# Performance work log

Measured on AMD Instinct MI355X. Metric: run time of the kernel, lower is better.

The kernel has to match this reference:

```python
import math
import jax, jax.numpy as jnp
import numpy as np

B, HRV, WRV, CRV = 1, 32, 512, 64
CBEV, HB, WB = 128, 256, 256
D, COUT, K, HEADS, P = 128, 128, 5, 8, 6
HD = D // HEADS
NBINS = 110
RMAX, BIN = 55.0, 0.5
XMIN, XMAX, YMIN, YMAX = -55.0, 55.0, -55.0, 55.0

_ELEV = np.array([-30.67, -29.33, -28.0, -26.66, -25.33, -24.0, -22.67, -21.33,
                  -20.0, -18.67, -17.33, -16.0, -14.67, -13.33, -12.0, -10.67,
                  -9.33, -8.0, -6.66, -5.33, -4.0, -2.67, -1.33, 0.0, 1.33,
                  2.67, 4.0, 5.33, 6.67, 8.0, 9.33, 10.67], dtype=np.float32)

def _make_uvec():
    az_line = np.linspace(-math.pi, math.pi, WRV + 1, dtype=np.float32)[:-1]
    az = az_line + 0.5 * (az_line[1] - az_line[0])
    elev = np.deg2rad(_ELEV[::-1].reshape(HRV, -1).mean(axis=1)).astype(np.float32)
    az2 = np.broadcast_to(az[None, :], (HRV, WRV))
    el2 = np.broadcast_to(elev[:, None], (HRV, WRV))
    ux = np.cos(az2) * np.cos(el2)
    uy = np.sin(az2) * np.cos(el2)
    uz = np.broadcast_to(np.sin(el2), (HRV, WRV))
    return jnp.asarray(ux), jnp.asarray(uy), jnp.asarray(uz)

_UX, _UY, _UZ = _make_uvec()

def _lin(x, w, b):
    # 1x1 conv / Linear: w is torch-layout [Cout, Cin]
    return jnp.einsum('...c,oc->...o', x, w) + b

def _gn(x, gamma, beta, groups, eps=1e-5):
    Bn, H, W, C = x.shape
    xg = x.reshape(Bn, H, W, groups, C // groups)
    mu = xg.mean(axis=(1, 2, 4), keepdims=True)
    var = ((xg - mu) ** 2).mean(axis=(1, 2, 4), keepdims=True)
    xg = (xg - mu) * jax.lax.rsqrt(var + eps)
    return xg.reshape(Bn, H, W, C) * gamma + beta

def _gelu(x):
    return jax.nn.gelu(x, approximate=False)

def _conv3x3_circ(x, w):
    # torch Conv2d(3x3, padding=1, padding_mode='circular', bias=False)
    xp = jnp.pad(x, ((0, 0), (1, 1), (1, 1), (0, 0)), mode='wrap')
    k = jnp.transpose(w, (2, 3, 1, 0))  # OIHW -> HWIO
    return jax.lax.conv_general_dilated(xp, k, (1, 1), 'VALID',
                                        dimension_numbers=('NHWC', 'HWIO', 'NHWC'))

def _deform_sample(v, loc, aw):
    # v: [B, HB*WB, HEADS, HD]; loc: [B,Nq,HEADS,P,2] normalized; aw: [B,Nq,HEADS,P]
    # Emulates grid_sample(bilinear, zeros padding, align_corners=False).
    Bq = v.shape[0]
    vflat = jnp.transpose(v, (0, 2, 1, 3))       # [B, H, HW, hd]
    loc_t = jnp.transpose(loc, (0, 2, 1, 3, 4))  # [B, H, Nq, P, 2]
    aw_t = jnp.transpose(aw, (0, 2, 1, 3))       # [B, H, Nq, P]
    x = loc_t[..., 0] * WB - 0.5
    y = loc_t[..., 1] * HB - 0.5
    x0 = jnp.floor(x); y0 = jnp.floor(y)
    wx1 = x - x0; wy1 = y - y0
    x0i = x0.astype(jnp.int32); y0i = y0.astype(jnp.int32)
    gather = jax.vmap(jax.vmap(lambda vf, idx: vf[idx]))  # over B, heads
    def corner(xi, yi, wgt, acc):
        valid = (xi >= 0) & (xi < WB) & (yi >= 0) & (yi < HB)
        idx = jnp.clip(yi, 0, HB - 1) * WB + jnp.clip(xi, 0, WB - 1)
        g = gather(vflat, idx)  # [B, H, Nq, P, hd]
        return acc + g * (wgt * valid.astype(g.dtype))[..., None]
    acc = jnp.zeros(x.shape + (HD,), dtype=v.dtype)
    acc = corner(x0i,     y0i,     (1 - wx1) * (1 - wy1), acc)
    acc = corner(x0i + 1, y0i,     wx1 * (1 - wy1), acc)
    acc = corner(x0i,     y0i + 1, (1 - wx1) * wy1, acc)
    acc = corner(x0i + 1, y0i + 1, wx1 * wy1, acc)
    out = (acc * aw_t[..., None]).sum(axis=3)    # [B, H, Nq, hd]
    return jnp.transpose(out, (0, 2, 1, 3)).reshape(Bq, -1, D)

def _forward(x_rv, bev, lidar2ego_mat, wq, bq, wv, bv, wo, bo,
             qd_w1, qd_b1, qd_w2, qd_b2,
             rh_w1, rh_b1, rh_g1, rh_be1, rh_w2, rh_g2, rh_be2, rh_w3, rh_b3,
             off_w, off_b, aw_w, aw_b, vp_w, vp_b, op_w, op_b):
    Bq = x_rv.shape[0]
    Q0 = _lin(x_rv, wq, bq)                                   # [B,Hrv,Wrv,D]
    Vmap = _lin(jnp.transpose(bev, (0, 2, 3, 1)), wv, bv)     # [B,HB,WB,D]
    uvec = jnp.broadcast_to(jnp.stack([_UX, _UY, _UZ], axis=-1)[None], (Bq, HRV, WRV, 3))
    h = _gelu(_gn(_lin(jnp.concatenate([x_rv, uvec], axis=-1), rh_w1, rh_b1), rh_g1, rh_be1, 8))
    h = _gelu(_gn(_conv3x3_circ(h, rh_w2), rh_g2, rh_be2, 8))
    depth_logits = _lin(h, rh_w3, rh_b3)                      # [B,Hrv,Wrv,NBINS]
    depth_dist = jax.nn.softmax(depth_logits, axis=-1)
    topk_prob, topk_idx = jax.lax.top_k(depth_dist, K)        # [B,Hrv,Wrv,K]
    topk_depths = jnp.minimum(BIN * (topk_idx.astype(jnp.float32) + 0.5), RMAX - 0.5 * BIN)
    xl = topk_depths * _UX[None, :, :, None]
    yl = topk_depths * _UY[None, :, :, None]
    zl = topk_depths * _UZ[None, :, :, None]
    p = jnp.stack([xl, yl, zl, jnp.ones_like(xl)], axis=-1)   # [B,Hrv,Wrv,K,4]
    pe = jnp.einsum('bhwki,ij->bhwkj', p, lidar2ego_mat[0])
    rx = (pe[..., 0] - XMIN) / (XMAX - XMIN)
    ry = (pe[..., 1] - YMIN) / (YMAX - YMIN)
    ref_pts = jnp.stack([jnp.clip(rx, 0.0, 1.0), jnp.clip(ry, 0.0, 1.0)], axis=-1).reshape(Bq, -1, 2)
    qin = jnp.concatenate([jnp.broadcast_to(Q0[:, :, :, None, :], (Bq, HRV, WRV, K, D)),
                           (topk_depths / RMAX)[..., None]], axis=-1)
    query = _lin(_gelu(_lin(qin, qd_w1, qd_b1)), qd_w2, qd_b2).reshape(Bq, -1, D)
    value = Vmap.reshape(Bq, -1, D)
    # --- MSDA (mmcv MultiScaleDeformableAttention, 1 level) ---
    v = _lin(value, vp_w, vp_b).reshape(Bq, -1, HEADS, HD)
    Nq = query.shape[1]
    off = _lin(query, off_w, off_b).reshape(Bq, Nq, HEADS, P, 2)
    aw = jax.nn.softmax(_lin(query, aw_w, aw_b).reshape(Bq, Nq, HEADS, P), axis=-1)
    loc = ref_pts[:, :, None, None, :] + off / jnp.array([WB, HB], dtype=jnp.float32)
    y_msda = _lin(_deform_sample(v, loc, aw), op_w, op_b) + query  # residual add
    y_msda = y_msda.reshape(Bq, HRV, WRV, K, D)
    wgt = topk_prob / (topk_prob.sum(axis=-1, keepdims=True) + 1e-8)
    y = (y_msda * wgt[..., None]).sum(axis=3)
    y = _lin(y, wo, bo)                                       # [B,Hrv,Wrv,COUT]
    return y, jnp.transpose(depth_logits, (0, 3, 1, 2))

def setup_inputs():
    key = jax.random.key(0)
    ks = jax.random.split(key, 32)
    def rn(i, shape, s):
        return jax.random.normal(ks[i], shape, dtype=jnp.float32) * s
    return dict(
        x_rv=rn(0, (B, HRV, WRV, CRV), 1.0),
        bev=rn(1, (B, CBEV, HB, WB), 1.0),
        lidar2ego_mat=jnp.eye(4, dtype=jnp.float32)[None] + rn(2, (1, 4, 4), 0.01),
        wq=rn(3, (D, CRV), 0.05), bq=rn(4, (D,), 0.01),
        wv=rn(5, (D, CBEV), 0.05), bv=rn(6, (D,), 0.01),
        wo=rn(7, (COUT, D), 0.05), bo=rn(8, (COUT,), 0.01),
        qd_w1=rn(9, (D, D + 1), 0.05), qd_b1=rn(10, (D,), 0.01),
        qd_w2=rn(11, (D, D), 0.05), qd_b2=rn(12, (D,), 0.01),
        rh_w1=rn(13, (128, CRV + 3), 0.05), rh_b1=rn(14, (128,), 0.01),
        rh_g1=jnp.ones((128,), jnp.float32), rh_be1=jnp.zeros((128,), jnp.float32),
        rh_w2=rn(15, (64, 128, 3, 3), 0.05),
        rh_g2=jnp.ones((64,), jnp.float32), rh_be2=jnp.zeros((64,), jnp.float32),
        rh_w3=rn(16, (NBINS, 64), 0.05), rh_b3=rn(17, (NBINS,), 0.01),
        off_w=rn(18, (HEADS * P * 2, D), 0.02), off_b=rn(19, (HEADS * P * 2,), 2.0),
        aw_w=rn(20, (HEADS * P, D), 0.02), aw_b=rn(21, (HEADS * P,), 0.01),
        vp_w=rn(22, (D, D), 0.05), vp_b=rn(23, (D,), 0.01),
        op_w=rn(24, (D, D), 0.05), op_b=rn(25, (D,), 0.01),
    )

def reference(x_rv, bev, lidar2ego_mat, wq, bq, wv, bv, wo, bo,
              qd_w1, qd_b1, qd_w2, qd_b2,
              rh_w1, rh_b1, rh_g1, rh_be1, rh_w2, rh_g2, rh_be2, rh_w3, rh_b3,
              off_w, off_b, aw_w, aw_b, vp_w, vp_b, op_w, op_b):
    return _forward(x_rv, bev, lidar2ego_mat, wq, bq, wv, bv, wo, bo,
                    qd_w1, qd_b1, qd_w2, qd_b2,
                    rh_w1, rh_b1, rh_g1, rh_be1, rh_w2, rh_g2, rh_be2, rh_w3, rh_b3,
                    off_w, off_b, aw_w, aw_b, vp_w, vp_b, op_w, op_b)
```

## Files before the change

kernel.cpp:

```cpp
#include <hip/hip_runtime.h>
#include <math.h>

#define NT 256

typedef unsigned short u16;
typedef unsigned int u32;
typedef _Float16 f16;
typedef __attribute__((ext_vector_type(2))) unsigned int u32x2;
typedef __attribute__((ext_vector_type(4))) unsigned int u32x4;
typedef __attribute__((ext_vector_type(4))) float f32x4;
typedef __attribute__((ext_vector_type(8))) short s16x8;
typedef __attribute__((ext_vector_type(8))) _Float16 f16x8;

namespace {

__device__ const float c_elev[32] = {
  -30.67f,-29.33f,-28.0f,-26.66f,-25.33f,-24.0f,-22.67f,-21.33f,
  -20.0f,-18.67f,-17.33f,-16.0f,-14.67f,-13.33f,-12.0f,-10.67f,
  -9.33f,-8.0f,-6.66f,-5.33f,-4.0f,-2.67f,-1.33f,0.0f,1.33f,
  2.67f,4.0f,5.33f,6.67f,8.0f,9.33f,10.67f };

__device__ __forceinline__ float gelu_f(float x) {
  return 0.5f * x * (1.0f + erff(x * 0.70710678118654752440f));
}
__device__ __forceinline__ u16 bf16rne(float f) {
  u32 u = __builtin_bit_cast(u32, f);
  u32 r = u + 0x7FFFu + ((u >> 16) & 1u);
  return (u16)(r >> 16);
}
__device__ __forceinline__ float bf2f(u16 h) {
  u32 u = ((u32)h) << 16;
  return __builtin_bit_cast(float, u);
}
__device__ __forceinline__ u32 packsplit(float x) {
  f16 h = (f16)x;
  f16 l = (f16)(x - (float)h);
  return (u32)__builtin_bit_cast(u16, h) | ((u32)__builtin_bit_cast(u16, l) << 16);
}
__device__ __forceinline__ void unpack16(u32x4 a, u32x4 b, f16x8& hi, f16x8& lo) {
  u32x4 h, l;
  h[0] = (a[0] & 0xFFFFu) | (a[1] << 16);  l[0] = (a[0] >> 16) | (a[1] & 0xFFFF0000u);
  h[1] = (a[2] & 0xFFFFu) | (a[3] << 16);  l[1] = (a[2] >> 16) | (a[3] & 0xFFFF0000u);
  h[2] = (b[0] & 0xFFFFu) | (b[1] << 16);  l[2] = (b[0] >> 16) | (b[1] & 0xFFFF0000u);
  h[3] = (b[2] & 0xFFFFu) | (b[3] << 16);  l[3] = (b[2] >> 16) | (b[3] & 0xFFFF0000u);
  hi = __builtin_bit_cast(f16x8, h);
  lo = __builtin_bit_cast(f16x8, l);
}

template<int COREAL, int CO, int KPAD, int CI, int PROD, int AMODE, bool DOGELU, bool OBF>
__global__ __launch_bounds__(NT)
void slin(const float* __restrict__ Af, const float* __restrict__ A2,
          const u32* __restrict__ Wp, const float* __restrict__ bias,
          float* __restrict__ outF, u16* __restrict__ outB)
{
  constexpr int BM = 64;
  constexpr int NFR = CO / 16;
  constexpr int KS = KPAD / 32;
  __shared__ u32 lds[BM * KPAD];
  const int tid = threadIdx.x;
  const long row0 = (long)blockIdx.x * BM;

  for (int i = tid; i < BM * (KPAD / 4); i += NT) {
    int r = i / (KPAD / 4), c = (i % (KPAD / 4)) * 4;
    long pix = row0 + r;
    u32x4 o;
    if constexpr (AMODE == 0) {
      if (c + 3 < CI) {
        f32x4 v = *(const f32x4*)(Af + pix * CI + c);
#pragma unroll
        for (int e = 0; e < 4; e++) o[e] = packsplit(v[e]);
      } else {
#pragma unroll
        for (int e = 0; e < 4; e++) {
          int cc = c + e;
          o[e] = packsplit(cc < CI ? Af[pix * CI + cc] : 0.f);
        }
      }
    } else {
      if (c + 3 < 64) {
        f32x4 v = *(const f32x4*)(Af + pix * 64 + c);
#pragma unroll
        for (int e = 0; e < 4; e++) o[e] = packsplit(v[e]);
      } else {
#pragma unroll
        for (int e = 0; e < 4; e++) {
          int cc = c + e;
          float x = (cc < 64) ? Af[pix * 64 + cc] : ((cc < 67) ? A2[pix * 3 + cc - 64] : 0.f);
          o[e] = packsplit(x);
        }
      }
    }
    *(u32x4*)((char*)lds + (((r * KPAD + c) * 4) ^ ((r & 7) << 4))) = o;
  }
  __syncthreads();

  const int wave = tid >> 6, lane = tid & 63;
  const int mb = wave * 16;
  const int lr = lane & 15, kq = lane >> 4;

  f32x4 acc[NFR] = {};
#pragma unroll
  for (int ks = 0; ks < KS; ks++) {
    const int arow = mb + lr;
    const u32 sw = (arow & 7) << 4;
    const int base = arow * KPAD * 4 + ks * 128 + kq * 32;
    u32x4 a0 = *(const u32x4*)((char*)lds + (base ^ sw));
    u32x4 a1 = *(const u32x4*)((char*)lds + ((base + 16) ^ sw));
    f16x8 ah, al;
    unpack16(a0, a1, ah, al);
#pragma unroll
    for (int nf = 0; nf < NFR; nf++) {
      const u32* wp = Wp + (nf * 16 + lr) * KPAD + ks * 32 + kq * 8;
      u32x4 w0 = *(const u32x4*)wp;
      u32x4 w1 = *(const u32x4*)(wp + 4);
      f16x8 wh, wl;
      unpack16(w0, w1, wh, wl);
      acc[nf] = __builtin_amdgcn_mfma_f32_16x16x32_f16(ah, wh, acc[nf], 0, 0, 0);
      if constexpr (PROD == 3) {
        acc[nf] = __builtin_amdgcn_mfma_f32_16x16x32_f16(ah, wl, acc[nf], 0, 0, 0);
        acc[nf] = __builtin_amdgcn_mfma_f32_16x16x32_f16(al, wh, acc[nf], 0, 0, 0);
      }
    }
  }

#pragma unroll
  for (int nf = 0; nf < NFR; nf++) {
    int col = nf * 16 + lr;
    if (col >= COREAL) continue;
    float bcol = bias[col];
#pragma unroll
    for (int r = 0; r < 4; r++) {
      long row = row0 + mb + kq * 4 + r;
      float val = acc[nf][r] + bcol;
      if constexpr (DOGELU) val = gelu_f(val);
      if constexpr (OBF) outB[row * COREAL + col] = bf16rne(val);
      else               outF[row * COREAL + col] = val;
    }
  }
}

__global__ __launch_bounds__(NT)
void conv_mfma(const float* __restrict__ X, const u32* __restrict__ Wc,
               float* __restrict__ Y)
{
  __shared__ u32 lds[4 * 18 * 128];
  const int tid = threadIdx.x;
  const int bRow = (blockIdx.x >> 5) * 2;
  const int bCol = (blockIdx.x & 31) * 16;

  for (int i = tid; i < 4 * 18 * 32; i += NT) {
    int c4 = (i & 31) * 4;
    int col = (i >> 5) % 18;
    int row = i / (18 * 32);
    int gy = (bRow + row - 1 + 32) & 31;
    int gx = (bCol + col - 1 + 512) & 511;
    f32x4 v = *(const f32x4*)(X + ((long)gy * 512 + gx) * 128 + c4);
    u32x4 o;
#pragma unroll
    for (int e = 0; e < 4; e++) o[e] = packsplit(v[e]);
    *(u32x4*)((char*)lds + ((((row * 18 + col) * 128 + c4) * 4) ^ ((col & 7) << 4))) = o;
  }
  __syncthreads();

  const int wave = tid >> 6, lane = tid & 63;
  const int wm = wave >> 1;
  const int nb = (wave & 1) * 32;
  const int lr = lane & 15, kq = lane >> 4;

  f32x4 acc[2] = {};
  for (int t = 0; t < 9; t++) {
    const int ky = t / 3, kx = t % 3;
    const int wrow = wm + ky;
    const int wcol = lr + kx;
    const u32 sw = (wcol & 7) << 4;
    const int rowbase = (wrow * 18 + wcol) * 512;
#pragma unroll
    for (int ks = 0; ks < 4; ks++) {
      const int base = rowbase + ks * 128 + kq * 32;
      u32x4 a0 = *(const u32x4*)((char*)lds + (base ^ sw));
      u32x4 a1 = *(const u32x4*)((char*)lds + ((base + 16) ^ sw));
      f16x8 ah, al;
      unpack16(a0, a1, ah, al);
#pragma unroll
      for (int nf = 0; nf < 2; nf++) {
        const u32* wp = Wc + ((t * 64 + nb + nf * 16 + lr) * 128 + ks * 32 + kq * 8);
        u32x4 w0 = *(const u32x4*)wp;
        u32x4 w1 = *(const u32x4*)(wp + 4);
        f16x8 wh, wl;
        unpack16(w0, w1, wh, wl);
        acc[nf] = __builtin_amdgcn_mfma_f32_16x16x32_f16(ah, wh, acc[nf], 0, 0, 0);
        acc[nf] = __builtin_amdgcn_mfma_f32_16x16x32_f16(ah, wl, acc[nf], 0, 0, 0);
        acc[nf] = __builtin_amdgcn_mfma_f32_16x16x32_f16(al, wh, acc[nf], 0, 0, 0);
      }
    }
  }

  const int gy = bRow + wm;
#pragma unroll
  for (int nf = 0; nf < 2; nf++) {
    int co = nb + nf * 16 + lr;
#pragma unroll
    for (int r = 0; r < 4; r++) {
      int gx = bCol + kq * 4 + r;
      Y[((long)gy * 512 + gx) * 64 + co] = acc[nf][r];
    }
  }
}

template<int CO, int AMODE, bool DEPTH, bool DOGELU, bool RESID, bool WF, bool WBF>
__global__ __launch_bounds__(NT)
void mfma_lin(const void* __restrict__ Ap, const float* __restrict__ A2,
              const u16* __restrict__ Wb, const float* __restrict__ bias,
              const float* __restrict__ extraW, const u16* __restrict__ residB,
              float* __restrict__ outF, u16* __restrict__ outB, int ldA)
{
  constexpr int BM = 64;
  __shared__ u32x4 smem[(BM + CO) * 16];
  char* As = (char*)smem;
  char* Bs = (char*)smem + BM * 256;
  const int tid = threadIdx.x;
  const long row0 = (long)blockIdx.x * BM;

  for (int i = tid; i < CO * 16; i += NT) {
    int r = i >> 4, ck = i & 15;
    u32x4 v = ((const u32x4*)(Wb + r * 128))[ck];
    *(u32x4*)(Bs + ((r * 256 + ck * 16) ^ ((r & 7) << 4))) = v;
  }
  if constexpr (AMODE == 0 || AMODE == 1) {
    const u16* A = (const u16*)Ap;
    for (int i = tid; i < BM * 16; i += NT) {
      int r = i >> 4, ck = i & 15;
      long src = (AMODE == 1) ? ((row0 + r) / 5) : (row0 + r);
      u32x4 v = ((const u32x4*)(A + src * 128))[ck];
      *(u32x4*)(As + ((r * 256 + ck * 16) ^ ((r & 7) << 4))) = v;
    }
  } else if constexpr (AMODE == 3) {
    const u16* A = (const u16*)Ap;
    for (int i = tid; i < BM * 16; i += NT) {
      int r = i >> 4, ck = i & 15;
      long q = row0 + r;
      float s[8];
#pragma unroll
      for (int e = 0; e < 8; e++) s[e] = 0.f;
#pragma unroll
      for (int j = 0; j < 5; j++) {
        float w = A2[q * 5 + j];
        u32x4 v = ((const u32x4*)(A + (q * 5 + j) * 128))[ck];
        const u16* hv = (const u16*)&v;
#pragma unroll
        for (int e = 0; e < 8; e++) s[e] += w * bf2f(hv[e]);
      }
      u32x4 o;
#pragma unroll
      for (int e = 0; e < 4; e++)
        o[e] = (u32)bf16rne(s[2 * e]) | ((u32)bf16rne(s[2 * e + 1]) << 16);
      *(u32x4*)(As + ((r * 256 + ck * 16) ^ ((r & 7) << 4))) = o;
    }
  } else if constexpr (AMODE == 4) {
    const float* A = (const float*)Ap;
    for (int i = tid; i < 128 * 16; i += NT) {
      int k = i >> 4, rg = i & 15;
      f32x4 v = *(const f32x4*)(A + (long)k * ldA + row0 + rg * 4);
#pragma unroll
      for (int e = 0; e < 4; e++) {
        int r = rg * 4 + e;
        *(u16*)(As + ((r * 256 + k * 2) ^ ((r & 7) << 4))) = bf16rne(v[e]);
      }
    }
  }
  __syncthreads();

  constexpr int WROWS = (CO >= 96) ? 2 : 4;
  constexpr int WCOLS = 4 / WROWS;
  constexpr int MW = BM / WROWS;
  constexpr int NW = CO / WCOLS;
  constexpr int MFR = MW / 16;
  constexpr int NFR = NW / 16;
  const int wave = tid >> 6, lane = tid & 63;
  const int wm = wave / WCOLS, wn = wave % WCOLS;
  const int mb = wm * MW, nb = wn * NW;
  const int lr = lane & 15, kq = lane >> 4;

  f32x4 acc[MFR][NFR] = {};
#pragma unroll
  for (int ks = 0; ks < 4; ks++) {
    const int kof = (ks * 32 + kq * 8) * 2;
    s16x8 af[MFR], bfr[NFR];
#pragma unroll
    for (int mf = 0; mf < MFR; mf++) {
      int r = mb + mf * 16 + lr;
      af[mf] = *(const s16x8*)(As + ((r * 256 + kof) ^ ((r & 7) << 4)));
    }
#pragma unroll
    for (int nf = 0; nf < NFR; nf++) {
      int r = nb + nf * 16 + lr;
      bfr[nf] = *(const s16x8*)(Bs + ((r * 256 + kof) ^ ((r & 7) << 4)));
    }
#pragma unroll
    for (int mf = 0; mf < MFR; mf++)
#pragma unroll
      for (int nf = 0; nf < NFR; nf++)
        acc[mf][nf] = __builtin_amdgcn_mfma_f32_16x16x32_bf16(af[mf], bfr[nf], acc[mf][nf], 0, 0, 0);
  }

#pragma unroll
  for (int mf = 0; mf < MFR; mf++) {
#pragma unroll
    for (int nf = 0; nf < NFR; nf++) {
      const int col = nb + nf * 16 + lr;
      const float bcol = bias[col];
      float ew = 0.f;
      if constexpr (DEPTH) ew = extraW[col];
#pragma unroll
      for (int r = 0; r < 4; r++) {
        long row = row0 + mb + mf * 16 + kq * 4 + r;
        float val = acc[mf][nf][r] + bcol;
        if constexpr (DEPTH) val += ew * (A2[row] * (1.0f / 55.0f));
        if constexpr (RESID) val += bf2f(residB[row * 128 + col]);
        if constexpr (DOGELU) val = gelu_f(val);
        if constexpr (WF) outF[row * CO + col] = val;
        if constexpr (WBF) outB[row * CO + col] = bf16rne(val);
      }
    }
  }
}

__global__ void wcomb_kernel(const float* __restrict__ vp_w, const float* __restrict__ wv,
                             const float* __restrict__ vp_b, const float* __restrict__ bv,
                             u16* __restrict__ wc, float* __restrict__ bc)
{
  int o = blockIdx.x;
  int c = threadIdx.x;
  float s = 0.f;
  for (int m = 0; m < 128; m++) s += vp_w[o * 128 + m] * wv[m * 128 + c];
  wc[o * 128 + c] = bf16rne(s);
  if (c == 0) {
    float b = vp_b[o];
    for (int m = 0; m < 128; m++) b += vp_w[o * 128 + m] * bv[m];
    bc[o] = b;
  }
}

__global__ void cvtw_kernel(const float* __restrict__ qd_w1, const float* __restrict__ qd_w2,
                            const float* __restrict__ off_w, const float* __restrict__ aw_w,
                            const float* __restrict__ op_w, const float* __restrict__ wo,
                            u16* Wq1, u16* Wq2, u16* Woff, u16* Waw, u16* Wop, u16* Wwo,
                            float* w1last)
{
  int i = blockIdx.x * NT + threadIdx.x;
  if (i < 16384) {
    int r = i >> 7, c = i & 127;
    Wq1[i] = bf16rne(qd_w1[r * 129 + c]);
    Wq2[i] = bf16rne(qd_w2[i]);
    Wop[i] = bf16rne(op_w[i]);
    Wwo[i] = bf16rne(wo[i]);
  }
  if (i < 12288) Woff[i] = bf16rne(off_w[i]);
  if (i < 6144)  Waw[i]  = bf16rne(aw_w[i]);
  if (i < 128)   w1last[i] = qd_w1[i * 129 + 128];
}

__global__ void packw_kernel(const float* __restrict__ rh_w1, const float* __restrict__ rh_w3,
                             const float* __restrict__ wq, const float* __restrict__ rh_w2,
                             u32* Wh1, u32* Wlog, u32* Wq0, u32* Wcv)
{
  int i = blockIdx.x * NT + threadIdx.x;
  if (i < 128 * 96) {
    int r = i / 96, c = i % 96;
    Wh1[i] = packsplit(c < 67 ? rh_w1[r * 67 + c] : 0.f);
  }
  if (i < 112 * 64) {
    int r = i / 64, c = i % 64;
    Wlog[i] = packsplit(r < 110 ? rh_w3[r * 64 + c] : 0.f);
  }
  if (i < 128 * 64) Wq0[i] = packsplit(wq[i]);
  if (i < 9 * 64 * 128) {
    int t = i / (64 * 128), o = (i / 128) % 64, c = i % 128;
    Wcv[i] = packsplit(rh_w2[(o * 128 + c) * 9 + t]);
  }
}

__global__ void uvec_kernel(float* __restrict__ uvec)
{
  int pix = blockIdx.x * NT + threadIdx.x;
  if (pix >= 16384) return;
  int hr = pix >> 9;
  int w = pix & 511;
  float el = c_elev[31 - hr] * 0.017453292519943295f;
  float az = -3.14159265358979323846f + ((float)w + 0.5f) * (6.283185307179586477f / 512.0f);
  float ce = cosf(el);
  uvec[pix * 3 + 0] = cosf(az) * ce;
  uvec[pix * 3 + 1] = sinf(az) * ce;
  uvec[pix * 3 + 2] = sinf(el);
}

template<int C, int S>
__global__ __launch_bounds__(NT)
void gn_stats_kernel(const float* __restrict__ X, int Npix, float* __restrict__ gs)
{
  constexpr int PPB = NT / C;
  int tid = threadIdx.x;
  int c = tid % C;
  int psub = tid / C;
  float sum = 0.f, ss = 0.f;
  for (long pix = (long)blockIdx.x * PPB + psub; pix < Npix; pix += (long)gridDim.x * PPB) {
    float v = X[pix * C + c];
    sum += v; ss += v * v;
  }
  __shared__ float ls[8][2];
  if (tid < 16) ls[tid / 2][tid % 2] = 0.f;
  __syncthreads();
  int g = c / S;
  atomicAdd(&ls[g][0], sum);
  atomicAdd(&ls[g][1], ss);
  __syncthreads();
  if (tid < 16) atomicAdd(&gs[tid], ls[tid / 2][tid % 2]);
}

template<int C, int S>
__global__ void gn_apply_kernel(float* __restrict__ X, long total, int Npix,
                                const float* __restrict__ gs,
                                const float* __restrict__ gamma, const float* __restrict__ beta)
{
  float cnt = (float)Npix * (float)S;
  for (long i = (long)blockIdx.x * NT + threadIdx.x; i < total; i += (long)gridDim.x * NT) {
    int c = (int)(i % C);
    int g = c / S;
    float mu = gs[g * 2] / cnt;
    float var = gs[g * 2 + 1] / cnt - mu * mu;
    float v = (X[i] - mu) * rsqrtf(var + 1e-5f);
    v = v * gamma[c] + beta[c];
    X[i] = gelu_f(v);
  }
}

__global__ __launch_bounds__(NT)
void tlogits_kernel(const float* __restrict__ logits, float* __restrict__ out1)
{
  __shared__ float ls[128][111];
  int p0 = blockIdx.x * 128;
  for (int i = threadIdx.x; i < 128 * 110; i += NT) {
    int p = i / 110, c = i % 110;
    ls[p][c] = logits[(long)(p0 + p) * 110 + c];
  }
  __syncthreads();
  for (int i = threadIdx.x; i < 110 * 128; i += NT) {
    int c = i / 128, p = i % 128;
    out1[(long)c * 16384 + p0 + p] = ls[p][c];
  }
}

__global__ __launch_bounds__(NT)
void topk_kernel(const float* __restrict__ logits, float* __restrict__ depths,
                 float* __restrict__ wgt)
{
  int lane = threadIdx.x & 63;
  int pix = (blockIdx.x * NT + threadIdx.x) >> 6;
  const float* lr = logits + (long)pix * 110;
  float v0 = (lane < 110) ? lr[lane] : -1e30f;
  float v1 = (lane + 64 < 110) ? lr[lane + 64] : -1e30f;
  float m = fmaxf(v0, v1);
#pragma unroll
  for (int s = 32; s; s >>= 1) m = fmaxf(m, __shfl_xor(m, s));
  float ex = ((lane < 110) ? expf(v0 - m) : 0.f) + ((lane + 64 < 110) ? expf(v1 - m) : 0.f);
  float den = ex;
#pragma unroll
  for (int s = 32; s; s >>= 1) den += __shfl_xor(den, s);
  float pr[5]; int pi[5];
#pragma unroll
  for (int j = 0; j < 5; j++) {
    float bv; int bi;
    if (v0 >= v1) { bv = v0; bi = lane; } else { bv = v1; bi = lane + 64; }
    for (int s = 1; s < 64; s <<= 1) {
      float ov = __shfl_xor(bv, s);
      int oi = __shfl_xor(bi, s);
      if (ov > bv || (ov == bv && oi < bi)) { bv = ov; bi = oi; }
    }
    pr[j] = expf(bv - m) / den;
    pi[j] = bi;
    if (bi == lane) v0 = -1e30f;
    if (bi == lane + 64) v1 = -1e30f;
  }
  if (lane == 0) {
    float tot = pr[0] + pr[1] + pr[2] + pr[3] + pr[4] + 1e-8f;
#pragma unroll
    for (int j = 0; j < 5; j++) {
      depths[pix * 5 + j] = fminf(0.5f * ((float)pi[j] + 0.5f), 54.75f);
      wgt[pix * 5 + j] = pr[j] / tot;
    }
  }
}

__global__ void refq_kernel(const float* __restrict__ depths, const float* __restrict__ uvec,
                            const float* __restrict__ L44, float* __restrict__ refq)
{
  long q = (long)blockIdx.x * NT + threadIdx.x;
  if (q >= 81920) return;
  long pix = q / 5;
  float d = depths[q];
  float px = d * uvec[pix * 3 + 0];
  float py = d * uvec[pix * 3 + 1];
  float pz = d * uvec[pix * 3 + 2];
  float pex = px * L44[0] + py * L44[4] + pz * L44[8] + L44[12];
  float pey = px * L44[1] + py * L44[5] + pz * L44[9] + L44[13];
  float rx = (pex + 55.0f) / 110.0f;
  float ry = (pey + 55.0f) / 110.0f;
  refq[q * 2 + 0] = fminf(fmaxf(rx, 0.f), 1.f);
  refq[q * 2 + 1] = fminf(fmaxf(ry, 0.f), 1.f);
}

__global__ __launch_bounds__(NT)
void msda_kernel(const u16* __restrict__ V, const float* __restrict__ refq,
                 const float* __restrict__ offb, const u16* __restrict__ awb,
                 u16* __restrict__ S)
{
  const int tid = threadIdx.x;
  const int kk = blockIdx.x >> 11;
  const int pg = blockIdx.x & 2047;
  const long pix = (long)pg * 8 + (tid >> 5);
  const long q = pix * 5 + kk;
  const int h = (tid >> 2) & 7;
  const int t4 = tid & 3;
  const int c0 = h * 16 + t4 * 4;
  const float rx = refq[q * 2 + 0], ry = refq[q * 2 + 1];
  const u16* ap = awb + q * 48 + h * 6;
  float a[6];
#pragma unroll
  for (int p = 0; p < 6; p++) a[p] = bf2f(ap[p]);
  float mx = fmaxf(fmaxf(fmaxf(a[0], a[1]), fmaxf(a[2], a[3])), fmaxf(a[4], a[5]));
  float se = 0.f;
#pragma unroll
  for (int p = 0; p < 6; p++) { a[p] = expf(a[p] - mx); se += a[p]; }
  float inv = 1.0f / se;
  const float* op = offb + q * 96 + h * 12;
  float acc0 = 0.f, acc1 = 0.f, acc2 = 0.f, acc3 = 0.f;
#pragma unroll
  for (int p = 0; p < 6; p++) {
    float x = (rx + op[p * 2 + 0] * (1.0f / 256.0f)) * 256.0f - 0.5f;
    float y = (ry + op[p * 2 + 1] * (1.0f / 256.0f)) * 256.0f - 0.5f;
    float x0f = floorf(x), y0f = floorf(y);
    float wx = x - x0f, wy = y - y0f;
    int x0 = (int)x0f, y0 = (int)y0f;
    float aw = a[p] * inv;
    float s0 = 0.f, s1 = 0.f, s2 = 0.f, s3 = 0.f;
#pragma unroll
    for (int cy = 0; cy < 2; cy++) {
#pragma unroll
      for (int cx = 0; cx < 2; cx++) {
        int xi = x0 + cx, yi = y0 + cy;
        float w = (cx ? wx : 1.f - wx) * (cy ? wy : 1.f - wy);
        bool valid = ((unsigned)xi < 256u) && ((unsigned)yi < 256u);
        int xc = min(max(xi, 0), 255), yc = min(max(yi, 0), 255);
        u32x2 v = *(const u32x2*)(V + (yc * 256 + xc) * 128 + c0);
        float w2 = valid ? w : 0.f;
        s0 += w2 * bf2f((u16)v[0]);
        s1 += w2 * bf2f((u16)(v[0] >> 16));
        s2 += w2 * bf2f((u16)v[1]);
        s3 += w2 * bf2f((u16)(v[1] >> 16));
      }
    }
    acc0 += aw * s0; acc1 += aw * s1; acc2 += aw * s2; acc3 += aw * s3;
  }
  u32x2 o;
  o[0] = (u32)bf16rne(acc0) | ((u32)bf16rne(acc1) << 16);
  o[1] = (u32)bf16rne(acc2) | ((u32)bf16rne(acc3) << 16);
  *(u32x2*)(S + q * 128 + c0) = o;
}

}

extern "C" void kernel_launch(void* const* d_in, const int* in_sizes, int n_in,
                              void* d_out, int out_size, void* d_ws, size_t ws_size,
                              hipStream_t stream)
{
  (void)in_sizes; (void)n_in; (void)out_size; (void)ws_size;
  const float* x_rv   = (const float*)d_in[0];
  const float* bev    = (const float*)d_in[1];
  const float* L44    = (const float*)d_in[2];
  const float* wq     = (const float*)d_in[3];
  const float* bq     = (const float*)d_in[4];
  const float* wv     = (const float*)d_in[5];
  const float* bv     = (const float*)d_in[6];
  const float* woW    = (const float*)d_in[7];
  const float* boB    = (const float*)d_in[8];
  const float* qd_w1  = (const float*)d_in[9];
  const float* qd_b1  = (const float*)d_in[10];
  const float* qd_w2  = (const float*)d_in[11];
  const float* qd_b2  = (const float*)d_in[12];
  const float* rh_w1  = (const float*)d_in[13];
  const float* rh_b1  = (const float*)d_in[14];
  const float* rh_g1  = (const float*)d_in[15];
  const float* rh_be1 = (const float*)d_in[16];
  const float* rh_w2  = (const float*)d_in[17];
  const float* rh_g2  = (const float*)d_in[18];
  const float* rh_be2 = (const float*)d_in[19];
  const float* rh_w3  = (const float*)d_in[20];
  const float* rh_b3  = (const float*)d_in[21];
  const float* off_w  = (const float*)d_in[22];
  const float* off_b  = (const float*)d_in[23];
  const float* aw_w   = (const float*)d_in[24];
  const float* aw_b   = (const float*)d_in[25];
  const float* vp_w   = (const float*)d_in[26];
  const float* vp_b   = (const float*)d_in[27];
  const float* op_w   = (const float*)d_in[28];
  const float* op_b   = (const float*)d_in[29];

  float* outY = (float*)d_out;
  float* outL = (float*)d_out + 2097152;

  char* wsb = (char*)d_ws;
  size_t off = 0;
  auto alloc = [&](size_t bytes) -> char* {
    char* p = wsb + off;
    off += (bytes + 255) & ~(size_t)255;
    return p;
  };

  u16*   wcomb  = (u16*)alloc(32768);
  float* bcomb  = (float*)alloc(512);
  float* uvec   = (float*)alloc(196608);
  float* stats  = (float*)alloc(128);
  float* depths = (float*)alloc(327680);
  float* wgtb   = (float*)alloc(327680);
  float* refqb  = (float*)alloc(655360);
  float* w1last = (float*)alloc(512);
  u16*   Wq1    = (u16*)alloc(32768);
  u16*   Wq2    = (u16*)alloc(32768);
  u16*   Wop    = (u16*)alloc(32768);
  u16*   Wwo    = (u16*)alloc(32768);
  u16*   Woff   = (u16*)alloc(24576);
  u16*   Waw    = (u16*)alloc(12288);
  u32*   Wh1    = (u32*)alloc(49152);
  u32*   Wlog   = (u32*)alloc(28672);
  u32*   Wq0    = (u32*)alloc(32768);
  u32*   Wcv    = (u32*)alloc(294912);
  char*  S1     = alloc(20971520);
  char*  S2     = alloc(4194304);
  char*  S3     = alloc(16777216);
  char*  S4     = alloc(20971520);
  char*  S5     = alloc(20971520);
  float* offbuf = (float*)alloc(31457280);
  u16*   awbf   = (u16*)alloc(7864320);

  float* h1buf  = (float*)S1;
  float* logits = (float*)(S1 + 8388608);
  float* h2buf  = (float*)(S1 + 15597568);
  u16*   smp    = (u16*)S1;
  u16*   Q0bf   = (u16*)S2;
  u16*   vbuf   = (u16*)S3;
  u16*   q1bf   = (u16*)S4;
  u16*   msdabf = (u16*)S4;
  u16*   querybf= (u16*)S5;

  float* stats1 = stats;
  float* stats2 = stats + 16;

  hipMemsetAsync((void*)stats, 0, 128, stream);

  wcomb_kernel<<<128, 128, 0, stream>>>(vp_w, wv, vp_b, bv, wcomb, bcomb);
  uvec_kernel<<<64, NT, 0, stream>>>(uvec);
  cvtw_kernel<<<64, NT, 0, stream>>>(qd_w1, qd_w2, off_w, aw_w, op_w, woW,
                                     Wq1, Wq2, Woff, Waw, Wop, Wwo, w1last);
  packw_kernel<<<288, NT, 0, stream>>>(rh_w1, rh_w3, wq, rh_w2, Wh1, Wlog, Wq0, Wcv);

  slin<128, 128, 64, 64, 1, 0, false, true><<<256, NT, 0, stream>>>(
      x_rv, nullptr, Wq0, bq, nullptr, Q0bf);

  slin<128, 128, 96, 67, 3, 1, false, false><<<256, NT, 0, stream>>>(
      x_rv, uvec, Wh1, rh_b1, h1buf, nullptr);
  gn_stats_kernel<128, 16><<<512, NT, 0, stream>>>(h1buf, 16384, stats1);
  gn_apply_kernel<128, 16><<<2048, NT, 0, stream>>>(h1buf, 16384L * 128, 16384, stats1, rh_g1, rh_be1);
  conv_mfma<<<512, NT, 0, stream>>>(h1buf, Wcv, h2buf);
  gn_stats_kernel<64, 8><<<512, NT, 0, stream>>>(h2buf, 16384, stats2);
  gn_apply_kernel<64, 8><<<1024, NT, 0, stream>>>(h2buf, 16384L * 64, 16384, stats2, rh_g2, rh_be2);
  slin<110, 112, 64, 64, 3, 0, false, false><<<256, NT, 0, stream>>>(
      h2buf, nullptr, Wlog, rh_b3, logits, nullptr);
  tlogits_kernel<<<128, NT, 0, stream>>>(logits, outL);
  topk_kernel<<<4096, NT, 0, stream>>>(logits, depths, wgtb);
  refq_kernel<<<320, NT, 0, stream>>>(depths, uvec, L44, refqb);

  mfma_lin<128, 4, false, false, false, false, true><<<1024, NT, 0, stream>>>(
      bev, nullptr, wcomb, bcomb, nullptr, nullptr, nullptr, vbuf, 65536);

  mfma_lin<128, 1, true, true, false, false, true><<<1280, NT, 0, stream>>>(
      Q0bf, depths, Wq1, qd_b1, w1last, nullptr, nullptr, q1bf, 0);
  mfma_lin<128, 0, false, false, false, false, true><<<1280, NT, 0, stream>>>(
      q1bf, nullptr, Wq2, qd_b2, nullptr, nullptr, nullptr, querybf, 0);

  mfma_lin<96, 0, false, false, false, true, false><<<1280, NT, 0, stream>>>(
      querybf, nullptr, Woff, off_b, nullptr, nullptr, offbuf, nullptr, 0);
  mfma_lin<48, 0, false, false, false, false, true><<<1280, NT, 0, stream>>>(
      querybf, nullptr, Waw, aw_b, nullptr, nullptr, nullptr, awbf, 0);

  msda_kernel<<<10240, NT, 0, stream>>>(vbuf, refqb, offbuf, awbf, smp);

  mfma_lin<128, 0, false, false, true, false, true><<<1280, NT, 0, stream>>>(
      smp, nullptr, Wop, op_b, nullptr, querybf, nullptr, msdabf, 0);

  mfma_lin<128, 3, false, false, false, true, false><<<256, NT, 0, stream>>>(
      msdabf, wgtb, Wwo, boB, nullptr, nullptr, outY, nullptr, 0);
}
```

Baseline: 430.8 us.

## Merge offset/attn GEMMs, fold output proj into final GEMM, widen MSDA threads

Merges the offset and attention-weight projections into one 160-column GEMM with a split epilogue. It uses linearity to move the weighted 5-candidate reduction ahead of the output projection. The op_w·wo product is precomputed, and a single K=256 GEMM over the concatenated reduced samples and query replaces two full-size GEMMs. The MSDA kernel now has each thread handle 16 channels of one head with 128-bit loads. The aim is fewer launches and less intermediate traffic, at the cost of changed bf16 rounding order and more registers per thread in MSDA.

```diff
diff --git a/kernel.cpp b/kernel.cpp
--- a/kernel.cpp
+++ b/kernel.cpp
@@ -31,6 +31,12 @@
 __device__ __forceinline__ float bf2f(u16 h) {
   u32 u = ((u32)h) << 16;
   return __builtin_bit_cast(float, u);
+}
+__device__ __forceinline__ float bflo(u32 v) {
+  return __builtin_bit_cast(float, v << 16);
+}
+__device__ __forceinline__ float bfhi(u32 v) {
+  return __builtin_bit_cast(float, v & 0xFFFF0000u);
 }
 __device__ __forceinline__ u32 packsplit(float x) {
   f16 h = (f16)x;
@@ -207,11 +213,11 @@
   }
 }
 
-template<int CO, int AMODE, bool DEPTH, bool DOGELU, bool RESID, bool WF, bool WBF>
+template<int CO, int AMODE, bool DEPTH, bool DOGELU, bool WF, bool WBF, bool SPLIT>
 __global__ __launch_bounds__(NT)
 void mfma_lin(const void* __restrict__ Ap, const float* __restrict__ A2,
               const u16* __restrict__ Wb, const float* __restrict__ bias,
-              const float* __restrict__ extraW, const u16* __restrict__ residB,
+              const float* __restrict__ extraW,
               float* __restrict__ outF, u16* __restrict__ outB, int ldA)
 {
   constexpr int BM = 64;
@@ -233,28 +239,6 @@
       long src = (AMODE == 1) ? ((row0 + r) / 5) : (row0 + r);
       u32x4 v = ((const u32x4*)(A + src * 128))[ck];
       *(u32x4*)(As + ((r * 256 + ck * 16) ^ ((r & 7) << 4))) = v;
-    }
-  } else if constexpr (AMODE == 3) {
-    const u16* A = (const u16*)Ap;
-    for (int i = tid; i < BM * 16; i += NT) {
-      int r = i >> 4, ck = i & 15;
-      long q = row0 + r;
-      float s[8];
-#pragma unroll
-      for (int e = 0; e < 8; e++) s[e] = 0.f;
-#pragma unroll
-      for (int j = 0; j < 5; j++) {
-        float w = A2[q * 5 + j];
-        u32x4 v = ((const u32x4*)(A + (q * 5 + j) * 128))[ck];
-        const u16* hv = (const u16*)&v;
-#pragma unroll
-        for (int e = 0; e < 8; e++) s[e] += w * bf2f(hv[e]);
-      }
-      u32x4 o;
-#pragma unroll
-      for (int e = 0; e < 4; e++)
-        o[e] = (u32)bf16rne(s[2 * e]) | ((u32)bf16rne(s[2 * e + 1]) << 16);
-      *(u32x4*)(As + ((r * 256 + ck * 16) ^ ((r & 7) << 4))) = o;
     }
   } else if constexpr (AMODE == 4) {
     const float* A = (const float*)Ap;
@@ -316,13 +300,95 @@
         long row = row0 + mb + mf * 16 + kq * 4 + r;
         float val = acc[mf][nf][r] + bcol;
         if constexpr (DEPTH) val += ew * (A2[row] * (1.0f / 55.0f));
-        if constexpr (RESID) val += bf2f(residB[row * 128 + col]);
         if constexpr (DOGELU) val = gelu_f(val);
-        if constexpr (WF) outF[row * CO + col] = val;
-        if constexpr (WBF) outB[row * CO + col] = bf16rne(val);
+        if constexpr (SPLIT) {
+          if (col < 96) outF[row * 96 + col] = val;
+          else if (col < 144) outB[row * 48 + (col - 96)] = bf16rne(val);
+        } else {
+          if constexpr (WF) outF[row * CO + col] = val;
+          if constexpr (WBF) outB[row * CO + col] = bf16rne(val);
+        }
       }
     }
   }
+}
+
+__global__ __launch_bounds__(NT)
+void final_gemm(const u16* __restrict__ A, const u16* __restrict__ Wc,
+                const float* __restrict__ cvec, float* __restrict__ outY)
+{
+  __shared__ char As[64 * 512];
+  const int tid = threadIdx.x;
+  const long row0 = (long)blockIdx.x * 64;
+  for (int i = tid; i < 64 * 32; i += NT) {
+    int r = i >> 5, ck = i & 31;
+    u32x4 v = ((const u32x4*)(A + (row0 + r) * 256))[ck];
+    *(u32x4*)(As + ((r * 512 + ck * 16) ^ ((r & 7) << 4))) = v;
+  }
+  __syncthreads();
+  const int wave = tid >> 6, lane = tid & 63;
+  const int mb = wave * 16;
+  const int lr = lane & 15, kq = lane >> 4;
+  f32x4 acc[8] = {};
+#pragma unroll
+  for (int ks = 0; ks < 8; ks++) {
+    const int kof = (ks * 32 + kq * 8) * 2;
+    const int r = mb + lr;
+    s16x8 af = *(const s16x8*)(As + ((r * 512 + kof) ^ ((r & 7) << 4)));
+#pragma unroll
+    for (int nf = 0; nf < 8; nf++) {
+      s16x8 bfr = *(const s16x8*)(Wc + (nf * 16 + lr) * 256 + ks * 32 + kq * 8);
+      acc[nf] = __builtin_amdgcn_mfma_f32_16x16x32_bf16(af, bfr, acc[nf], 0, 0, 0);
+    }
+  }
+#pragma unroll
+  for (int nf = 0; nf < 8; nf++) {
+    int col = nf * 16 + lr;
+    float bcol = cvec[col];
+#pragma unroll
+    for (int r = 0; r < 4; r++) {
+      long row = row0 + mb + kq * 4 + r;
+      outY[row * 128 + col] = acc[nf][r] + bcol;
+    }
+  }
+}
+
+__global__ __launch_bounds__(NT)
+void combine_kernel(const u16* __restrict__ smp, const u16* __restrict__ query,
+                    const float* __restrict__ wgt, u16* __restrict__ acat)
+{
+  const long idx = (long)blockIdx.x * NT + threadIdx.x;
+  const long pix = idx >> 3;
+  const int c0 = (idx & 7) * 16;
+  float w[5];
+#pragma unroll
+  for (int k = 0; k < 5; k++) w[k] = wgt[pix * 5 + k];
+  float as[16] = {}, aq[16] = {};
+#pragma unroll
+  for (int k = 0; k < 5; k++) {
+    const u32x4* sp = (const u32x4*)(smp + (pix * 5 + k) * 128 + c0);
+    const u32x4* qp = (const u32x4*)(query + (pix * 5 + k) * 128 + c0);
+    u32x4 s0 = sp[0], s1 = sp[1], q0 = qp[0], q1 = qp[1];
+#pragma unroll
+    for (int e = 0; e < 4; e++) {
+      as[2 * e]     += w[k] * bflo(s0[e]);  as[2 * e + 1] += w[k] * bfhi(s0[e]);
+      as[8 + 2 * e] += w[k] * bflo(s1[e]);  as[9 + 2 * e] += w[k] * bfhi(s1[e]);
+      aq[2 * e]     += w[k] * bflo(q0[e]);  aq[2 * e + 1] += w[k] * bfhi(q0[e]);
+      aq[8 + 2 * e] += w[k] * bflo(q1[e]);  aq[9 + 2 * e] += w[k] * bfhi(q1[e]);
+    }
+  }
+  u32x4 o0, o1, o2, o3;
+#pragma unroll
+  for (int e = 0; e < 4; e++) {
+    o0[e] = (u32)bf16rne(as[2 * e]) | ((u32)bf16rne(as[2 * e + 1]) << 16);
+    o1[e] = (u32)bf16rne(as[8 + 2 * e]) | ((u32)bf16rne(as[9 + 2 * e]) << 16);
+    o2[e] = (u32)bf16rne(aq[2 * e]) | ((u32)bf16rne(aq[2 * e + 1]) << 16);
+    o3[e] = (u32)bf16rne(aq[8 + 2 * e]) | ((u32)bf16rne(aq[9 + 2 * e]) << 16);
+  }
+  u32x4* dst = (u32x4*)(acat + pix * 256 + c0);
+  dst[0] = o0; dst[1] = o1;
+  u32x4* dst2 = (u32x4*)(acat + pix * 256 + 128 + c0);
+  dst2[0] = o2; dst2[1] = o3;
 }
 
 __global__ void wcomb_kernel(const float* __restrict__ vp_w, const float* __restrict__ wv,
@@ -341,23 +407,41 @@
   }
 }
 
+__global__ void wopcomb_kernel(const float* __restrict__ wo, const float* __restrict__ op_w,
+                               const float* __restrict__ op_b, const float* __restrict__ bo,
+                               u16* __restrict__ Wcat, float* __restrict__ cvec)
+{
+  int o = blockIdx.x;
+  int c = threadIdx.x;
+  float s = 0.f;
+  for (int m = 0; m < 128; m++) s += wo[o * 128 + m] * op_w[m * 128 + c];
+  Wcat[o * 256 + c] = bf16rne(s);
+  Wcat[o * 256 + 128 + c] = bf16rne(wo[o * 128 + c]);
+  if (c == 0) {
+    float b = bo[o];
+    for (int m = 0; m < 128; m++) b += wo[o * 128 + m] * op_b[m];
+    cvec[o] = b;
+  }
+}
+
 __global__ void cvtw_kernel(const float* __restrict__ qd_w1, const float* __restrict__ qd_w2,
                             const float* __restrict__ off_w, const float* __restrict__ aw_w,
-                            const float* __restrict__ op_w, const float* __restrict__ wo,
-                            u16* Wq1, u16* Wq2, u16* Woff, u16* Waw, u16* Wop, u16* Wwo,
-                            float* w1last)
+                            const float* __restrict__ off_b, const float* __restrict__ aw_b,
+                            u16* Wq1, u16* Wq2, u16* Wmg, float* mgbias, float* w1last)
 {
   int i = blockIdx.x * NT + threadIdx.x;
   if (i < 16384) {
     int r = i >> 7, c = i & 127;
     Wq1[i] = bf16rne(qd_w1[r * 129 + c]);
     Wq2[i] = bf16rne(qd_w2[i]);
-    Wop[i] = bf16rne(op_w[i]);
-    Wwo[i] = bf16rne(wo[i]);
-  }
-  if (i < 12288) Woff[i] = bf16rne(off_w[i]);
-  if (i < 6144)  Waw[i]  = bf16rne(aw_w[i]);
-  if (i < 128)   w1last[i] = qd_w1[i * 129 + 128];
+  }
+  if (i < 20480) {
+    int r = i >> 7, c = i & 127;
+    float v = (r < 96) ? off_w[r * 128 + c] : ((r < 144) ? aw_w[(r - 96) * 128 + c] : 0.f);
+    Wmg[i] = bf16rne(v);
+  }
+  if (i < 160) mgbias[i] = (i < 96) ? off_b[i] : ((i < 144) ? aw_b[i - 96] : 0.f);
+  if (i < 128) w1last[i] = qd_w1[i * 129 + 128];
 }
 
 __global__ void packw_kernel(const float* __restrict__ rh_w1, const float* __restrict__ rh_w3,
@@ -515,56 +599,72 @@
                  u16* __restrict__ S)
 {
   const int tid = threadIdx.x;
-  const int kk = blockIdx.x >> 11;
-  const int pg = blockIdx.x & 2047;
-  const long pix = (long)pg * 8 + (tid >> 5);
+  const int kk = blockIdx.x >> 9;
+  const int pg = blockIdx.x & 511;
+  const long pix = (long)pg * 32 + (tid >> 3);
+  const int h = tid & 7;
   const long q = pix * 5 + kk;
-  const int h = (tid >> 2) & 7;
-  const int t4 = tid & 3;
-  const int c0 = h * 16 + t4 * 4;
+  const int c0 = h * 16;
   const float rx = refq[q * 2 + 0], ry = refq[q * 2 + 1];
-  const u16* ap = awb + q * 48 + h * 6;
-  float a[6];
-#pragma unroll
-  for (int p = 0; p < 6; p++) a[p] = bf2f(ap[p]);
+
+  const u32* ap32 = (const u32*)(awb + q * 48 + h * 6);
+  u32 aw0 = ap32[0], aw1 = ap32[1], aw2 = ap32[2];
+  float a[6] = { bflo(aw0), bfhi(aw0), bflo(aw1), bfhi(aw1), bflo(aw2), bfhi(aw2) };
   float mx = fmaxf(fmaxf(fmaxf(a[0], a[1]), fmaxf(a[2], a[3])), fmaxf(a[4], a[5]));
   float se = 0.f;
 #pragma unroll
-  for (int p = 0; p < 6; p++) { a[p] = expf(a[p] - mx); se += a[p]; }
-  float inv = 1.0f / se;
-  const float* op = offb + q * 96 + h * 12;
-  float acc0 = 0.f, acc1 = 0.f, acc2 = 0.f, acc3 = 0.f;
+  for (int p = 0; p < 6; p++) { a[p] = __expf(a[p] - mx); se += a[p]; }
+  const float inv = 1.0f / se;
+
+  const f32x4* opv = (const f32x4*)(offb + q * 96 + h * 12);
+  f32x4 of0 = opv[0], of1 = opv[1], of2 = opv[2];
+  const float ox[6] = { of0[0], of0[2], of1[0], of1[2], of2[0], of2[2] };
+  const float oy[6] = { of0[1], of0[3], of1[1], of1[3], of2[1], of2[3] };
+
+  float acc[16];
+#pragma unroll
+  for (int j = 0; j < 16; j++) acc[j] = 0.f;
+
 #pragma unroll
   for (int p = 0; p < 6; p++) {
-    float x = (rx + op[p * 2 + 0] * (1.0f / 256.0f)) * 256.0f - 0.5f;
-    float y = (ry + op[p * 2 + 1] * (1.0f / 256.0f)) * 256.0f - 0.5f;
+    float x = (rx + ox[p] * (1.0f / 256.0f)) * 256.0f - 0.5f;
+    float y = (ry + oy[p] * (1.0f / 256.0f)) * 256.0f - 0.5f;
     float x0f = floorf(x), y0f = floorf(y);
     float wx = x - x0f, wy = y - y0f;
-    int x0 = (int)x0f, y0 = (int)y0f;
-    float aw = a[p] * inv;
-    float s0 = 0.f, s1 = 0.f, s2 = 0.f, s3 = 0.f;
+    int ix = (int)x0f, iy = (int)y0f;
+    float awp = a[p] * inv;
+    float wx0 = ((unsigned)ix < 256u) ? (1.f - wx) : 0.f;
+    float wx1 = ((unsigned)(ix + 1) < 256u) ? wx : 0.f;
+    float wy0 = ((unsigned)iy < 256u) ? (awp * (1.f - wy)) : 0.f;
+    float wy1 = ((unsigned)(iy + 1) < 256u) ? (awp * wy) : 0.f;
+    int xc0 = min(max(ix, 0), 255), xc1 = min(max(ix + 1, 0), 255);
+    int yc0 = min(max(iy, 0), 255), yc1 = min(max(iy + 1, 0), 255);
 #pragma unroll
     for (int cy = 0; cy < 2; cy++) {
+      int yc = cy ? yc1 : yc0;
+      float wyv = cy ? wy1 : wy0;
 #pragma unroll
       for (int cx = 0; cx < 2; cx++) {
-        int xi = x0 + cx, yi = y0 + cy;
-        float w = (cx ? wx : 1.f - wx) * (cy ? wy : 1.f - wy);
-        bool valid = ((unsigned)xi < 256u) && ((unsigned)yi < 256u);
-        int xc = min(max(xi, 0), 255), yc = min(max(yi, 0), 255);
-        u32x2 v = *(const u32x2*)(V + (yc * 256 + xc) * 128 + c0);
-        float w2 = valid ? w : 0.f;
-        s0 += w2 * bf2f((u16)v[0]);
-        s1 += w2 * bf2f((u16)(v[0] >> 16));
-        s2 += w2 * bf2f((u16)v[1]);
-        s3 += w2 * bf2f((u16)(v[1] >> 16));
+        int xc = cx ? xc1 : xc0;
+        float m = (cx ? wx1 : wx0) * wyv;
+        const u32x4* vp = (const u32x4*)(V + (yc * 256 + xc) * 128 + c0);
+        u32x4 v0 = vp[0], v1 = vp[1];
+#pragma unroll
+        for (int e = 0; e < 4; e++) {
+          acc[2 * e]     += m * bflo(v0[e]);  acc[2 * e + 1] += m * bfhi(v0[e]);
+          acc[8 + 2 * e] += m * bflo(v1[e]);  acc[9 + 2 * e] += m * bfhi(v1[e]);
+        }
       }
     }
-    acc0 += aw * s0; acc1 += aw * s1; acc2 += aw * s2; acc3 += aw * s3;
-  }
-  u32x2 o;
-  o[0] = (u32)bf16rne(acc0) | ((u32)bf16rne(acc1) << 16);
-  o[1] = (u32)bf16rne(acc2) | ((u32)bf16rne(acc3) << 16);
-  *(u32x2*)(S + q * 128 + c0) = o;
+  }
+  u32x4 o0, o1;
+#pragma unroll
+  for (int e = 0; e < 4; e++) {
+    o0[e] = (u32)bf16rne(acc[2 * e]) | ((u32)bf16rne(acc[2 * e + 1]) << 16);
+    o1[e] = (u32)bf16rne(acc[8 + 2 * e]) | ((u32)bf16rne(acc[9 + 2 * e]) << 16);
+  }
+  u32x4* dst = (u32x4*)(S + q * 128 + c0);
+  dst[0] = o0; dst[1] = o1;
 }
 
 }
@@ -626,10 +726,10 @@
   float* w1last = (float*)alloc(512);
   u16*   Wq1    = (u16*)alloc(32768);
   u16*   Wq2    = (u16*)alloc(32768);
-  u16*   Wop    = (u16*)alloc(32768);
-  u16*   Wwo    = (u16*)alloc(32768);
-  u16*   Woff   = (u16*)alloc(24576);
-  u16*   Waw    = (u16*)alloc(12288);
+  u16*   Wmg    = (u16*)alloc(40960);
+  float* mgbias = (float*)alloc(640);
+  u16*   Wcat   = (u16*)alloc(65536);
+  float* cvec   = (float*)alloc(512);
   u32*   Wh1    = (u32*)alloc(49152);
   u32*   Wlog   = (u32*)alloc(28672);
   u32*   Wq0    = (u32*)alloc(32768);
@@ -649,7 +749,7 @@
   u16*   Q0bf   = (u16*)S2;
   u16*   vbuf   = (u16*)S3;
   u16*   q1bf   = (u16*)S4;
-  u16*   msdabf = (u16*)S4;
+  u16*   acat   = (u16*)S4;
   u16*   querybf= (u16*)S5;
 
   float* stats1 = stats;
@@ -658,9 +758,10 @@
   hipMemsetAsync((void*)stats, 0, 128, stream);
 
   wcomb_kernel<<<128, 128, 0, stream>>>(vp_w, wv, vp_b, bv, wcomb, bcomb);
+  wopcomb_kernel<<<128, 128, 0, stream>>>(woW, op_w, op_b, boB, Wcat, cvec);
   uvec_kernel<<<64, NT, 0, stream>>>(uvec);
-  cvtw_kernel<<<64, NT, 0, stream>>>(qd_w1, qd_w2, off_w, aw_w, op_w, woW,
-                                     Wq1, Wq2, Woff, Waw, Wop, Wwo, w1last);
+  cvtw_kernel<<<80, NT, 0, stream>>>(qd_w1, qd_w2, off_w, aw_w, off_b, aw_b,
+                                     Wq1, Wq2, Wmg, mgbias, w1last);
   packw_kernel<<<288, NT, 0, stream>>>(rh_w1, rh_w3, wq, rh_w2, Wh1, Wlog, Wq0, Wcv);
 
   slin<128, 128, 64, 64, 1, 0, false, true><<<256, NT, 0, stream>>>(
@@ -679,24 +780,20 @@
   topk_kernel<<<4096, NT, 0, stream>>>(logits, depths, wgtb);
   refq_kernel<<<320, NT, 0, stream>>>(depths, uvec, L44, refqb);
 
-  mfma_lin<128, 4, false, false, false, false, true><<<1024, NT, 0, stream>>>(
-      bev, nullptr, wcomb, bcomb, nullptr, nullptr, nullptr, vbuf, 65536);
-
-  mfma_lin<128, 1, true, true, false, false, true><<<1280, NT, 0, stream>>>(
-      Q0bf, depths, Wq1, qd_b1, w1last, nullptr, nullptr, q1bf, 0);
-  mfma_lin<128, 0, false, false, false, false, true><<<1280, NT, 0, stream>>>(
-      q1bf, nullptr, Wq2, qd_b2, nullptr, nullptr, nullptr, querybf, 0);
-
-  mfma_lin<96, 0, false, false, false, true, false><<<1280, NT, 0, stream>>>(
-      querybf, nullptr, Woff, off_b, nullptr, nullptr, offbuf, nullptr, 0);
-  mfma_lin<48, 0, false, false, false, false, true><<<1280, NT, 0, stream>>>(
-      querybf, nullptr, Waw, aw_b, nullptr, nullptr, nullptr, awbf, 0);
-
-  msda_kernel<<<10240, NT, 0, stream>>>(vbuf, refqb, offbuf, awbf, smp);
-
-  mfma_lin<128, 0, false, false, true, false, true><<<1280, NT, 0, stream>>>(
-      smp, nullptr, Wop, op_b, nullptr, querybf, nullptr, msdabf, 0);
-
-  mfma_lin<128, 3, false, false, false, true, false><<<256, NT, 0, stream>>>(
-      msdabf, wgtb, Wwo, boB, nullptr, nullptr, outY, nullptr, 0);
-}
+  mfma_lin<128, 4, false, false, false, true, false><<<1024, NT, 0, stream>>>(
+      bev, nullptr, wcomb, bcomb, nullptr, nullptr, vbuf, 65536);
+
+  mfma_lin<128, 1, true, true, false, true, false><<<1280, NT, 0, stream>>>(
+      Q0bf, depths, Wq1, qd_b1, w1last, nullptr, q1bf, 0);
+  mfma_lin<128, 0, false, false, false, true, false><<<1280, NT, 0, stream>>>(
+      q1bf, nullptr, Wq2, qd_b2, nullptr, nullptr, querybf, 0);
+
+  mfma_lin<160, 0, false, false, false, false, true><<<1280, NT, 0, stream>>>(
+      querybf, nullptr, Wmg, mgbias, nullptr, offbuf, awbf, 0);
+
+  msda_kernel<<<2560, NT, 0, stream>>>(vbuf, refqb, offbuf, awbf, smp);
+
+  combine_kernel<<<512, NT, 0, stream>>>(smp, querybf, wgtb, acat);
+
+  final_gemm<<<256, NT, 0, stream>>>(acat, Wcat, cvec, outY);
+}
```

Result: slower. 452.3 us (+5.0%).
